# Kernel tuning notes

Hardware: AMD Instinct MI355X
Metric: run time of the kernel (lower is better)

## Reference

```python
import jax, jax.numpy as jnp
import numpy as np

K = 3
STRIDE = 1
PAD = 1
C_IN = 256
C_OUT = 256
BN_EPS = 1e-5


def conv2d(x, w, b, stride, pad):
    # x: (N,C,H,W), w: (O,I,K,K)
    y = jax.lax.conv_general_dilated(
        x, w, window_strides=(stride, stride),
        padding=((pad, pad), (pad, pad)),
        dimension_numbers=("NCHW", "OIHW", "NCHW"))
    return y + b[None, :, None, None]


def deform_conv2d(x, offset, weight, stride, pad, k):
    # torchvision-style deformable conv v1 (no modulation, no bias),
    # offset layout: (N, 2*k*k, Ho, Wo) with (dy, dx) pairs per kernel tap.
    N, C, H, W = x.shape
    Ho, Wo = offset.shape[2], offset.shape[3]
    KK = k * k
    off = offset.reshape(N, KK, 2, Ho, Wo)
    dy, dx = off[:, :, 0], off[:, :, 1]                      # (N,KK,Ho,Wo)

    ky, kx = jnp.meshgrid(jnp.arange(k), jnp.arange(k), indexing="ij")
    ky = ky.reshape(1, KK, 1, 1).astype(x.dtype)
    kx = kx.reshape(1, KK, 1, 1).astype(x.dtype)
    base_y = (jnp.arange(Ho) * stride - pad).astype(x.dtype)[None, None, :, None]
    base_x = (jnp.arange(Wo) * stride - pad).astype(x.dtype)[None, None, None, :]

    py = base_y + ky + dy                                     # (N,KK,Ho,Wo)
    px = base_x + kx + dx

    y0 = jnp.floor(py)
    x0 = jnp.floor(px)
    ly = py - y0
    lx = px - x0
    y0i = y0.astype(jnp.int32)
    x0i = x0.astype(jnp.int32)

    x_flat = x.reshape(N, C, H * W)

    def gather(yi, xi):
        valid = (yi >= 0) & (yi < H) & (xi >= 0) & (xi < W)
        yc = jnp.clip(yi, 0, H - 1)
        xc = jnp.clip(xi, 0, W - 1)
        idx = yc * W + xc                                     # (N,KK,Ho,Wo)
        v = jax.vmap(lambda xf, i: xf[:, i])(x_flat, idx)     # (N,C,KK,Ho,Wo)
        return v * valid[:, None].astype(x.dtype)

    w_tl = ((1 - ly) * (1 - lx))[:, None]
    w_tr = ((1 - ly) * lx)[:, None]
    w_bl = (ly * (1 - lx))[:, None]
    w_br = (ly * lx)[:, None]

    val = (w_tl * gather(y0i, x0i) + w_tr * gather(y0i, x0i + 1)
           + w_bl * gather(y0i + 1, x0i) + w_br * gather(y0i + 1, x0i + 1))
    # val: (N, Ci, KK, Ho, Wo); weight: (Co, Ci, k, k)
    w2 = weight.reshape(weight.shape[0], weight.shape[1], KK)
    return jnp.einsum("bikhw,oik->bohw", val, w2)


def setup_inputs() -> dict:
    key = jax.random.key(0)
    k1, k2, k3, k4 = jax.random.split(key, 4)
    N, H, W = 8, 64, 64
    x = jax.random.normal(k1, (N, C_IN, H, W), dtype=jnp.float32)
    # small nonzero offset-conv weights so the deformable gather is exercised
    w_offset = jax.random.normal(k2, (2 * K * K, C_IN, K, K), dtype=jnp.float32) * 0.01
    b_offset = jax.random.normal(k3, (2 * K * K,), dtype=jnp.float32) * 0.1
    w_conv = jax.random.normal(k4, (C_OUT, C_IN, K, K), dtype=jnp.float32) / np.sqrt(C_IN * K * K)
    gamma = jnp.ones((C_OUT,), dtype=jnp.float32)
    beta = jnp.zeros((C_OUT,), dtype=jnp.float32)
    return {"x": x, "w_offset": w_offset, "b_offset": b_offset,
            "w_conv": w_conv, "gamma": gamma, "beta": beta}


def reference(x, w_offset, b_offset, w_conv, gamma, beta):
    offset = conv2d(x, w_offset, b_offset, STRIDE, PAD)
    out = deform_conv2d(x, offset, w_conv, STRIDE, PAD, K)
    # BatchNorm2d in training mode: batch stats over (N,H,W), biased variance
    mean = jnp.mean(out, axis=(0, 2, 3), keepdims=True)
    var = jnp.mean(jnp.square(out - mean), axis=(0, 2, 3), keepdims=True)
    out = (out - mean) * jax.lax.rsqrt(var + BN_EPS)
    out = out * gamma[None, :, None, None] + beta[None, :, None, None]
    return out * jax.nn.sigmoid(out)  # SiLU
```

## Files before the change

### kernel.cpp

```cpp
#include <hip/hip_runtime.h>
#include <math.h>

#define HW 4096
#define KTOT 2304

typedef __attribute__((ext_vector_type(8))) short short8v;
typedef __attribute__((ext_vector_type(4))) float float4v;

__device__ __forceinline__ unsigned int bf16rne(float f) {
  unsigned int x = __float_as_uint(f);
  return (x + 0x7fffu + ((x >> 16) & 1u)) >> 16;
}

__device__ __forceinline__ unsigned int bilin_pack(unsigned int u0, unsigned int u1,
                                                   unsigned int u2, unsigned int u3,
                                                   float w0, float w1, float w2, float w3) {
  float lo = w0 * __uint_as_float(u0 << 16) + w1 * __uint_as_float(u1 << 16) +
             w2 * __uint_as_float(u2 << 16) + w3 * __uint_as_float(u3 << 16);
  float hi = w0 * __uint_as_float(u0 & 0xFFFF0000u) + w1 * __uint_as_float(u1 & 0xFFFF0000u) +
             w2 * __uint_as_float(u2 & 0xFFFF0000u) + w3 * __uint_as_float(u3 & 0xFFFF0000u);
  unsigned int r;
  asm("v_cvt_pk_bf16_f32 %0, %1, %2" : "=v"(r) : "v"(lo), "v"(hi));
  return r;
}


__global__ __launch_bounds__(256) void k_tx_prep(const float* __restrict__ x,
                                                 const float* __restrict__ wc,
                                                 const float* __restrict__ wo,
                                                 ushort* __restrict__ xT,
                                                 ushort* __restrict__ wB,
                                                 ushort* __restrict__ wOB) {
  int bid = blockIdx.x;
  if (bid < 512) {
    int n = bid & 7, p0 = (bid >> 3) << 6;
    int t = threadIdx.x;
    int lane = t & 63, wave = t >> 6, c0 = wave << 6;
    const float* xb = x + ((size_t)(n * 256 + c0)) * HW + p0 + lane;
    ushort* ob = xT + ((size_t)n * 4096 + p0 + lane) * 256 + c0;
#pragma unroll
    for (int g = 0; g < 8; ++g) {
      unsigned int u[4];
#pragma unroll
      for (int j = 0; j < 4; ++j) {
        float v0 = xb[(size_t)(g * 8 + 2 * j) * HW];
        float v1 = xb[(size_t)(g * 8 + 2 * j + 1) * HW];
        u[j] = bf16rne(v0) | (bf16rne(v1) << 16);
      }
      *reinterpret_cast<uint4*>(ob + g * 8) = make_uint4(u[0], u[1], u[2], u[3]);
    }
  } else if (bid < 800) {
    int t = (bid - 512) * 256 + threadIdx.x;
    int ks = t >> 10;
    int l = t & 63;
    int of = (t >> 6) & 15;
    int kk = ks >> 3;
    int cbase = ((ks & 7) << 5) + ((l >> 4) << 3);
    int oc = (of << 4) + (l & 15);
    unsigned int u[8];
#pragma unroll
    for (int j = 0; j < 8; ++j)
      u[j] = bf16rne(wc[(size_t)oc * KTOT + (size_t)(cbase + j) * 9 + kk]);
    *reinterpret_cast<uint4*>(&wB[(size_t)t * 8]) =
        make_uint4(u[0] | (u[1] << 16), u[2] | (u[3] << 16),
                   u[4] | (u[5] << 16), u[6] | (u[7] << 16));
  } else {
    int t = (bid - 800) * 256 + threadIdx.x;
    int ks = t >> 7;
    int l = t & 63;
    int of = (t >> 6) & 1;
    int kk = ks >> 3;
    int cbase = ((ks & 7) << 5) + ((l >> 4) << 3);
    int oc = (of << 4) + (l & 15);
    unsigned int u[8];
#pragma unroll
    for (int j = 0; j < 8; ++j)
      u[j] = (oc < 18) ? bf16rne(wo[(size_t)oc * KTOT + (size_t)(cbase + j) * 9 + kk]) : 0u;
    *reinterpret_cast<uint4*>(&wOB[(size_t)t * 8]) =
        make_uint4(u[0] | (u[1] << 16), u[2] | (u[3] << 16),
                   u[4] | (u[5] << 16), u[6] | (u[7] << 16));
  }
}

__global__ __launch_bounds__(512, 4) void k_offset5(
    const ushort* __restrict__ xT, const ushort* __restrict__ wOffB,
    const float* __restrict__ b_off, float* __restrict__ off_out) {
  __shared__ ushort s_tile[2][64 * 64];

  int bid = blockIdx.x;
  int n = bid & 7, ho = bid >> 3;
  int t = threadIdx.x;
  int lane = t & 63, wave = t >> 6;
  int coct = lane & 7;
  int p = (wave << 3) + (lane >> 3);
  int ocf = wave & 1, pixf = wave >> 1;

  const ushort* xTn = xT + (size_t)n * 4096 * 256;

  float4v acc = (float4v)0.f;

  auto srcp = [&](int kk, const ushort*& s, bool& v) {
    int ky = kk / 3, kx = kk - ky * 3;
    int oy = ho + ky - 1, ox = p + kx - 1;
    v = (oy >= 0) & (oy < 64) & (ox >= 0) & (ox < 64);
    s = xTn + (size_t)(oy * 64 + ox) * 256 + (coct << 3);
  };

  auto issue = [&](uint4& a, const ushort* s, bool v, int cg) {
    a = v ? *reinterpret_cast<const uint4*>(s + (cg << 6)) : make_uint4(0, 0, 0, 0);
  };

  auto step = [&](uint4 a, int ksb, int buf) {
    short8v wf[2];
#pragma unroll
    for (int ks2 = 0; ks2 < 2; ++ks2)
      wf[ks2] = *reinterpret_cast<const short8v*>(
          &wOffB[(((size_t)((ksb + ks2) * 2 + ocf)) * 64 + lane) * 8]);
    *reinterpret_cast<uint4*>(&s_tile[buf][p * 64 + ((coct ^ (p & 7)) << 3)]) = a;
    asm volatile("s_waitcnt lgkmcnt(0)" ::: "memory");
    __builtin_amdgcn_s_barrier();
#pragma unroll
    for (int ks2 = 0; ks2 < 2; ++ks2) {
      int row = (pixf << 4) + (lane & 15);
      int g = (ks2 << 2) + (lane >> 4);
      int slot = g ^ (row & 7);
      short8v vf = *reinterpret_cast<const short8v*>(&s_tile[buf][row * 64 + slot * 8]);
      acc = __builtin_amdgcn_mfma_f32_16x16x32_bf16(wf[ks2], vf, acc, 0, 0, 0);
    }
  };

  const ushort* cs;
  bool cv;
  srcp(0, cs, cv);
  uint4 A, B;
  issue(A, cs, cv, 0);

  for (int kk = 0; kk < 9; ++kk) {
    int ksb = kk << 3;
    issue(B, cs, cv, 1);
    step(A, ksb + 0, 0);
    issue(A, cs, cv, 2);
    step(B, ksb + 2, 1);
    issue(B, cs, cv, 3);
    step(A, ksb + 4, 0);
    const ushort* ns = cs;
    bool nv = cv;
    if (kk < 8) {
      srcp(kk + 1, ns, nv);
      issue(A, ns, nv, 0);
    }
    step(B, ksb + 6, 1);
    cs = ns; cv = nv;
  }

  int pixcol = (pixf << 4) + (lane & 15);
  size_t base = ((size_t)n * 4096 + ho * 64 + pixcol) * 18;
#pragma unroll
  for (int j = 0; j < 4; ++j) {
    int oc = (ocf << 4) + ((lane >> 4) << 2) + j;
    if (oc < 18) off_out[base + oc] = acc[j] + b_off[oc];
  }
}

__global__ __launch_bounds__(512, 4) void k_deform10(
    const ushort* __restrict__ xT, const float* __restrict__ off,
    const ushort* __restrict__ wB, float* __restrict__ out,
    float2* __restrict__ part) {
  __shared__ ushort s_val[2][64 * 64];
  __shared__ int4   s_gi[9][64];
  __shared__ float4 s_gw[9][64];

  int bid = blockIdx.x;
  int n = bid & 7, ho = bid >> 3;
  int t = threadIdx.x;
  int lane = t & 63, wave = t >> 6;
  int coct = lane & 7;
  int p = (wave << 3) + (lane >> 3);

  const ushort* xTn = xT + (size_t)n * 4096 * 256;

  for (int e = t; e < 576; e += 512) {
    int pix = e & 63, kk = e >> 6;
    int ky = kk / 3, kx = kk - ky * 3;
    const float* ob = off + ((size_t)n * 4096 + ho * 64 + pix) * 18;
    float dy = ob[2 * kk], dx = ob[2 * kk + 1];
    float py = (float)(ho - 1 + ky) + dy;
    float px = (float)(pix - 1 + kx) + dx;
    float y0f = floorf(py), x0f = floorf(px);
    float ly = py - y0f, lx = px - x0f;
    int y0 = (int)y0f, x0 = (int)x0f;
    int y1 = y0 + 1, x1 = x0 + 1;
    float vy0 = (y0 >= 0 && y0 < 64) ? 1.f : 0.f;
    float vy1 = (y1 >= 0 && y1 < 64) ? 1.f : 0.f;
    float vx0 = (x0 >= 0 && x0 < 64) ? 1.f : 0.f;
    float vx1 = (x1 >= 0 && x1 < 64) ? 1.f : 0.f;
    int cy0 = min(max(y0, 0), 63) << 6, cy1 = min(max(y1, 0), 63) << 6;
    int cx0 = min(max(x0, 0), 63), cx1 = min(max(x1, 0), 63);
    s_gi[kk][pix] = make_int4((cy0 + cx0) << 8, (cy0 + cx1) << 8,
                              (cy1 + cx0) << 8, (cy1 + cx1) << 8);
    s_gw[kk][pix] = make_float4((1.f - ly) * (1.f - lx) * vy0 * vx0,
                                (1.f - ly) * lx * vy0 * vx1,
                                ly * (1.f - lx) * vy1 * vx0,
                                ly * lx * vy1 * vx1);
  }
  __syncthreads();

  float4v acc[2][4];
#pragma unroll
  for (int a = 0; a < 2; ++a)
#pragma unroll
    for (int b = 0; b < 4; ++b) acc[a][b] = (float4v)0.f;

  uint4 TA[4], TB[4];

  auto issue = [&](uint4 (&T)[4], int kk, int cg) {
    int4 g = s_gi[kk][p];
    int cb = (cg << 6) + (coct << 3);
    T[0] = *reinterpret_cast<const uint4*>(xTn + g.x + cb);
    T[1] = *reinterpret_cast<const uint4*>(xTn + g.y + cb);
    T[2] = *reinterpret_cast<const uint4*>(xTn + g.z + cb);
    T[3] = *reinterpret_cast<const uint4*>(xTn + g.w + cb);
  };

  auto step = [&](uint4 (&T)[4], int kk, int ks0, int buf) {
    short8v wf[2][2];
#pragma unroll
    for (int ks2 = 0; ks2 < 2; ++ks2)
#pragma unroll
      for (int mf = 0; mf < 2; ++mf)
        wf[ks2][mf] = *reinterpret_cast<const short8v*>(
            &wB[(((size_t)((ks0 + ks2) * 16 + (wave << 1) + mf)) * 64 + lane) * 8]);
    float4 w = s_gw[kk][p];
    uint4 r;
    r.x = bilin_pack(T[0].x, T[1].x, T[2].x, T[3].x, w.x, w.y, w.z, w.w);
    r.y = bilin_pack(T[0].y, T[1].y, T[2].y, T[3].y, w.x, w.y, w.z, w.w);
    r.z = bilin_pack(T[0].z, T[1].z, T[2].z, T[3].z, w.x, w.y, w.z, w.w);
    r.w = bilin_pack(T[0].w, T[1].w, T[2].w, T[3].w, w.x, w.y, w.z, w.w);
    *reinterpret_cast<uint4*>(&s_val[buf][p * 64 + ((coct ^ (p & 7)) << 3)]) = r;
    asm volatile("s_waitcnt lgkmcnt(0)" ::: "memory");
    __builtin_amdgcn_s_barrier();
    __builtin_amdgcn_s_setprio(1);
#pragma unroll
    for (int ks2 = 0; ks2 < 2; ++ks2) {
#pragma unroll
      for (int pf = 0; pf < 4; ++pf) {
        int row = (pf << 4) + (lane & 15);
        int g = (ks2 << 2) + (lane >> 4);
        int slot = g ^ (row & 7);
        short8v vf = *reinterpret_cast<const short8v*>(&s_val[buf][row * 64 + slot * 8]);
#pragma unroll
        for (int mf = 0; mf < 2; ++mf)
          acc[mf][pf] = __builtin_amdgcn_mfma_f32_16x16x32_bf16(
              wf[ks2][mf], vf, acc[mf][pf], 0, 0, 0);
      }
    }
    __builtin_amdgcn_s_setprio(0);
  };

  issue(TA, 0, 0);
  for (int kk = 0; kk < 9; ++kk) {
    int ks0 = kk << 3;
    issue(TB, kk, 1);
    step(TA, kk, ks0 + 0, 0);
    issue(TA, kk, 2);
    step(TB, kk, ks0 + 2, 1);
    issue(TB, kk, 3);
    step(TA, kk, ks0 + 4, 0);
    if (kk < 8) issue(TA, kk + 1, 0);
    step(TB, kk, ks0 + 6, 1);
  }

#pragma unroll
  for (int mf = 0; mf < 2; ++mf) {
    int ocb = (wave << 5) + (mf << 4) + ((lane >> 4) << 2);
#pragma unroll
    for (int pf = 0; pf < 4; ++pf) {
      int wo = (pf << 4) + (lane & 15);
      float* op = out + (((size_t)(n * 256 + ocb)) * 64 + ho) * 64 + wo;
      float4v a = acc[mf][pf];
      op[0] = a[0];
      op[HW] = a[1];
      op[2 * HW] = a[2];
      op[3 * HW] = a[3];
    }
  }
  float s[2][4], q[2][4];
#pragma unroll
  for (int mf = 0; mf < 2; ++mf)
#pragma unroll
    for (int j = 0; j < 4; ++j) {
      float ss = 0.f, qq = 0.f;
#pragma unroll
      for (int pf = 0; pf < 4; ++pf) {
        float v = acc[mf][pf][j];
        ss += v;
        qq += v * v;
      }
      s[mf][j] = ss;
      q[mf][j] = qq;
    }
#pragma unroll
  for (int o = 1; o < 16; o <<= 1) {
#pragma unroll
    for (int mf = 0; mf < 2; ++mf)
#pragma unroll
      for (int j = 0; j < 4; ++j) {
        s[mf][j] += __shfl_xor(s[mf][j], o);
        q[mf][j] += __shfl_xor(q[mf][j], o);
      }
  }
  if ((lane & 15) == 0) {
#pragma unroll
    for (int mf = 0; mf < 2; ++mf)
#pragma unroll
      for (int j = 0; j < 4; ++j) {
        int oc = (wave << 5) + (mf << 4) + ((lane >> 4) << 2) + j;
        part[(size_t)oc * 512 + bid] = make_float2(s[mf][j], q[mf][j]);
      }
  }
}

__global__ __launch_bounds__(256) void k_stats_fin(const float2* __restrict__ part,
                                                   float2* __restrict__ stats) {
  int oc = blockIdx.x;
  int t = threadIdx.x;
  float2 a = part[(size_t)oc * 512 + t];
  float2 b = part[(size_t)oc * 512 + 256 + t];
  float s = a.x + b.x, q = a.y + b.y;
#pragma unroll
  for (int o = 32; o; o >>= 1) {
    s += __shfl_down(s, o);
    q += __shfl_down(q, o);
  }
  __shared__ float2 wsum[4];
  if ((t & 63) == 0) wsum[t >> 6] = make_float2(s, q);
  __syncthreads();
  if (t == 0) {
    float S = wsum[0].x + wsum[1].x + wsum[2].x + wsum[3].x;
    float Q = wsum[0].y + wsum[1].y + wsum[2].y + wsum[3].y;
    float mean = S / 32768.f;
    float var = Q / 32768.f - mean * mean;
    stats[oc] = make_float2(mean, rsqrtf(var + 1e-5f));
  }
}

__global__ __launch_bounds__(256) void k_bn_silu(float* __restrict__ out,
                                                 const float2* __restrict__ stats,
                                                 const float* __restrict__ gamma,
                                                 const float* __restrict__ beta) {
  int b = blockIdx.x;
  int nb = (b & 7) * 1024 + (b >> 3);
  size_t i4 = (size_t)nb * 256 + threadIdx.x;
  int ch = (int)((i4 >> 10) & 255);
  float2 st = stats[ch];
  float g = gamma[ch] * st.y;
  float bb = beta[ch] - st.x * g;
  float4 v = *(float4*)(out + i4 * 4);
  float y0 = v.x * g + bb, y1 = v.y * g + bb, y2 = v.z * g + bb, y3 = v.w * g + bb;
  v.x = y0 / (1.f + expf(-y0));
  v.y = y1 / (1.f + expf(-y1));
  v.z = y2 / (1.f + expf(-y2));
  v.w = y3 / (1.f + expf(-y3));
  *(float4*)(out + i4 * 4) = v;
}

extern "C" void kernel_launch(void* const* d_in, const int* in_sizes, int n_in,
                              void* d_out, int out_size, void* d_ws, size_t ws_size,
                              hipStream_t stream) {
  const float* x      = (const float*)d_in[0];
  const float* w_off  = (const float*)d_in[1];
  const float* b_off  = (const float*)d_in[2];
  const float* w_conv = (const float*)d_in[3];
  const float* gamma  = (const float*)d_in[4];
  const float* beta   = (const float*)d_in[5];
  float* out = (float*)d_out;

  float* ws       = (float*)d_ws;
  float*  ws_off  = ws;
  ushort* ws_xT   = (ushort*)(ws + 589824);
  ushort* ws_wB   = (ushort*)(ws + 4784128);
  ushort* ws_wOB  = (ushort*)(ws + 5079040);
  float2* ws_part = (float2*)(ws + 5115904);
  float2* ws_st   = (float2*)(ws + 5378048);

  k_tx_prep<<<836, 256, 0, stream>>>(x, w_conv, w_off, ws_xT, ws_wB, ws_wOB);
  k_offset5<<<512, 512, 0, stream>>>(ws_xT, ws_wOB, b_off, ws_off);
  k_deform10<<<512, 512, 0, stream>>>(ws_xT, ws_off, ws_wB, out, ws_part);
  k_stats_fin<<<256, 256, 0, stream>>>(ws_part, ws_st);
  k_bn_silu<<<8192, 256, 0, stream>>>(out, ws_st, gamma, beta);
}
```

Measured before the change: 108.4 us.

## Software-pipeline deform conv: pack next chunk while MFMAs consume previous buffer

Restructures the deformable-conv main loop into a flat 36-chunk pipeline. Each iteration packs bilinear values for chunk c into one LDS buffer while the MFMAs consume chunk c-1 from the other, with one barrier per chunk placed after both. Previously each step packed and then waited at a barrier before its own MFMAs. The aim is to overlap the gather/interpolation ALU work with matrix math and take the barrier wait off the critical path. The cost is more live registers and a prologue/epilogue.

Result: slower. 111.2 us (+2.5%).

```diff
diff --git a/kernel.cpp b/kernel.cpp
--- a/kernel.cpp
+++ b/kernel.cpp
@@ -162,7 +162,7 @@
   }
 }
 
-__global__ __launch_bounds__(512, 4) void k_deform10(
+__global__ __launch_bounds__(512, 4) void k_deform11(
     const ushort* __restrict__ xT, const float* __restrict__ off,
     const ushort* __restrict__ wB, float* __restrict__ out,
     float2* __restrict__ part) {
@@ -213,32 +213,26 @@
 
   uint4 TA[4], TB[4];
 
-  auto issue = [&](uint4 (&T)[4], int kk, int cg) {
-    int4 g = s_gi[kk][p];
-    int cb = (cg << 6) + (coct << 3);
+  auto issueT = [&](uint4 (&T)[4], int c) {
+    int4 g = s_gi[c >> 2][p];
+    int cb = ((c & 3) << 6) + (coct << 3);
     T[0] = *reinterpret_cast<const uint4*>(xTn + g.x + cb);
     T[1] = *reinterpret_cast<const uint4*>(xTn + g.y + cb);
     T[2] = *reinterpret_cast<const uint4*>(xTn + g.z + cb);
     T[3] = *reinterpret_cast<const uint4*>(xTn + g.w + cb);
   };
 
-  auto step = [&](uint4 (&T)[4], int kk, int ks0, int buf) {
-    short8v wf[2][2];
-#pragma unroll
-    for (int ks2 = 0; ks2 < 2; ++ks2)
-#pragma unroll
-      for (int mf = 0; mf < 2; ++mf)
-        wf[ks2][mf] = *reinterpret_cast<const short8v*>(
-            &wB[(((size_t)((ks0 + ks2) * 16 + (wave << 1) + mf)) * 64 + lane) * 8]);
-    float4 w = s_gw[kk][p];
+  auto pack = [&](uint4 (&T)[4], int c, int buf) {
+    float4 w = s_gw[c >> 2][p];
     uint4 r;
     r.x = bilin_pack(T[0].x, T[1].x, T[2].x, T[3].x, w.x, w.y, w.z, w.w);
     r.y = bilin_pack(T[0].y, T[1].y, T[2].y, T[3].y, w.x, w.y, w.z, w.w);
     r.z = bilin_pack(T[0].z, T[1].z, T[2].z, T[3].z, w.x, w.y, w.z, w.w);
     r.w = bilin_pack(T[0].w, T[1].w, T[2].w, T[3].w, w.x, w.y, w.z, w.w);
     *reinterpret_cast<uint4*>(&s_val[buf][p * 64 + ((coct ^ (p & 7)) << 3)]) = r;
-    asm volatile("s_waitcnt lgkmcnt(0)" ::: "memory");
-    __builtin_amdgcn_s_barrier();
+  };
+
+  auto mfma_exec = [&](short8v (&wf)[2][2], int buf) {
     __builtin_amdgcn_s_setprio(1);
 #pragma unroll
     for (int ks2 = 0; ks2 < 2; ++ks2) {
@@ -257,17 +251,47 @@
     __builtin_amdgcn_s_setprio(0);
   };
 
-  issue(TA, 0, 0);
-  for (int kk = 0; kk < 9; ++kk) {
-    int ks0 = kk << 3;
-    issue(TB, kk, 1);
-    step(TA, kk, ks0 + 0, 0);
-    issue(TA, kk, 2);
-    step(TB, kk, ks0 + 2, 1);
-    issue(TB, kk, 3);
-    step(TA, kk, ks0 + 4, 0);
-    if (kk < 8) issue(TA, kk + 1, 0);
-    step(TB, kk, ks0 + 6, 1);
+  auto load_wf = [&](short8v (&wf)[2][2], int m) {
+    int ks0 = m << 1;
+#pragma unroll
+    for (int ks2 = 0; ks2 < 2; ++ks2)
+#pragma unroll
+      for (int mf = 0; mf < 2; ++mf)
+        wf[ks2][mf] = *reinterpret_cast<const short8v*>(
+            &wB[(((size_t)((ks0 + ks2) * 16 + (wave << 1) + mf)) * 64 + lane) * 8]);
+  };
+
+  issueT(TA, 0);
+  issueT(TB, 1);
+  pack(TA, 0, 0);
+  asm volatile("s_waitcnt lgkmcnt(0)" ::: "memory");
+  __builtin_amdgcn_s_barrier();
+
+  for (int cc = 1; cc < 36; cc += 2) {
+    {
+      if (cc < 35) issueT(TA, cc + 1);
+      short8v wf[2][2];
+      load_wf(wf, cc - 1);
+      pack(TB, cc, 1);
+      mfma_exec(wf, 0);
+      asm volatile("s_waitcnt lgkmcnt(0)" ::: "memory");
+      __builtin_amdgcn_s_barrier();
+    }
+    if (cc + 1 < 36) {
+      if (cc + 2 < 36) issueT(TB, cc + 2);
+      short8v wf[2][2];
+      load_wf(wf, cc);
+      pack(TA, cc + 1, 0);
+      mfma_exec(wf, 1);
+      asm volatile("s_waitcnt lgkmcnt(0)" ::: "memory");
+      __builtin_amdgcn_s_barrier();
+    }
+  }
+
+  {
+    short8v wf[2][2];
+    load_wf(wf, 35);
+    mfma_exec(wf, 1);
   }
 
 #pragma unroll
@@ -385,7 +409,7 @@
 
   k_tx_prep<<<836, 256, 0, stream>>>(x, w_conv, w_off, ws_xT, ws_wB, ws_wOB);
   k_offset5<<<512, 512, 0, stream>>>(ws_xT, ws_wOB, b_off, ws_off);
-  k_deform10<<<512, 512, 0, stream>>>(ws_xT, ws_off, ws_wB, out, ws_part);
+  k_deform11<<<512, 512, 0, stream>>>(ws_xT, ws_off, ws_wB, out, ws_part);
   k_stats_fin<<<256, 256, 0, stream>>>(ws_part, ws_st);
   k_bn_silu<<<8192, 256, 0, stream>>>(out, ws_st, gamma, beta);
 }
```

## Stage two 64-channel chunks per barrier in deformable-conv main loop

Applied to the files above, without the earlier changes.

Restructures the deformable-conv main loop so each phase packs two 64-channel gathered tiles into a wider LDS buffer (128 channels per pixel) and runs two MFMA groups per barrier, halving the number of barriers from 36 to 18. It also issues gathers for the next phase before the current phase's weight loads and MFMAs, so global latency overlaps with compute. The cost is double the LDS for s_val (32 KB) and more live registers, which could lower occupancy under the 512x4 launch bound.

Result: no change. 108.6 us (+0.1%).

```diff
diff --git a/kernel.cpp b/kernel.cpp
--- a/kernel.cpp
+++ b/kernel.cpp
@@ -162,11 +162,11 @@
   }
 }
 
-__global__ __launch_bounds__(512, 4) void k_deform10(
+__global__ __launch_bounds__(512, 4) void k_deform12(
     const ushort* __restrict__ xT, const float* __restrict__ off,
     const ushort* __restrict__ wB, float* __restrict__ out,
     float2* __restrict__ part) {
-  __shared__ ushort s_val[2][64 * 64];
+  __shared__ ushort s_val[2][64 * 128];
   __shared__ int4   s_gi[9][64];
   __shared__ float4 s_gw[9][64];
 
@@ -213,33 +213,34 @@
 
   uint4 TA[4], TB[4];
 
-  auto issue = [&](uint4 (&T)[4], int kk, int cg) {
-    int4 g = s_gi[kk][p];
-    int cb = (cg << 6) + (coct << 3);
+  auto issueT = [&](uint4 (&T)[4], const int4& g, int c) {
+    int cb = ((c & 3) << 6) + (coct << 3);
     T[0] = *reinterpret_cast<const uint4*>(xTn + g.x + cb);
     T[1] = *reinterpret_cast<const uint4*>(xTn + g.y + cb);
     T[2] = *reinterpret_cast<const uint4*>(xTn + g.z + cb);
     T[3] = *reinterpret_cast<const uint4*>(xTn + g.w + cb);
   };
 
-  auto step = [&](uint4 (&T)[4], int kk, int ks0, int buf) {
-    short8v wf[2][2];
-#pragma unroll
-    for (int ks2 = 0; ks2 < 2; ++ks2)
-#pragma unroll
-      for (int mf = 0; mf < 2; ++mf)
-        wf[ks2][mf] = *reinterpret_cast<const short8v*>(
-            &wB[(((size_t)((ks0 + ks2) * 16 + (wave << 1) + mf)) * 64 + lane) * 8]);
-    float4 w = s_gw[kk][p];
+  auto pack = [&](uint4 (&T)[4], const float4& w, int c, int buf) {
     uint4 r;
     r.x = bilin_pack(T[0].x, T[1].x, T[2].x, T[3].x, w.x, w.y, w.z, w.w);
     r.y = bilin_pack(T[0].y, T[1].y, T[2].y, T[3].y, w.x, w.y, w.z, w.w);
     r.z = bilin_pack(T[0].z, T[1].z, T[2].z, T[3].z, w.x, w.y, w.z, w.w);
     r.w = bilin_pack(T[0].w, T[1].w, T[2].w, T[3].w, w.x, w.y, w.z, w.w);
-    *reinterpret_cast<uint4*>(&s_val[buf][p * 64 + ((coct ^ (p & 7)) << 3)]) = r;
-    asm volatile("s_waitcnt lgkmcnt(0)" ::: "memory");
-    __builtin_amdgcn_s_barrier();
-    __builtin_amdgcn_s_setprio(1);
+    *reinterpret_cast<uint4*>(
+        &s_val[buf][p * 128 + ((c & 1) << 6) + ((coct ^ (p & 7)) << 3)]) = r;
+  };
+
+  auto load_wf2 = [&](short8v (&wf)[2][2], int ksbase) {
+#pragma unroll
+    for (int ks2 = 0; ks2 < 2; ++ks2)
+#pragma unroll
+      for (int mf = 0; mf < 2; ++mf)
+        wf[ks2][mf] = *reinterpret_cast<const short8v*>(
+            &wB[(((size_t)((ksbase + ks2) * 16 + (wave << 1) + mf)) * 64 + lane) * 8]);
+  };
+
+  auto mfma2 = [&](short8v (&wf)[2][2], int buf, int half) {
 #pragma unroll
     for (int ks2 = 0; ks2 < 2; ++ks2) {
 #pragma unroll
@@ -247,27 +248,43 @@
         int row = (pf << 4) + (lane & 15);
         int g = (ks2 << 2) + (lane >> 4);
         int slot = g ^ (row & 7);
-        short8v vf = *reinterpret_cast<const short8v*>(&s_val[buf][row * 64 + slot * 8]);
+        short8v vf = *reinterpret_cast<const short8v*>(
+            &s_val[buf][row * 128 + (half << 6) + slot * 8]);
 #pragma unroll
         for (int mf = 0; mf < 2; ++mf)
           acc[mf][pf] = __builtin_amdgcn_mfma_f32_16x16x32_bf16(
               wf[ks2][mf], vf, acc[mf][pf], 0, 0, 0);
       }
     }
+  };
+
+  {
+    int4 g0 = s_gi[0][p];
+    issueT(TA, g0, 0);
+    issueT(TB, g0, 1);
+  }
+
+  for (int ph = 0; ph < 18; ++ph) {
+    int kk = ph >> 1;
+    int buf = ph & 1;
+    float4 w = s_gw[kk][p];
+    pack(TA, w, 2 * ph, buf);
+    pack(TB, w, 2 * ph + 1, buf);
+    if (ph < 17) {
+      int4 g = s_gi[(ph + 1) >> 1][p];
+      issueT(TA, g, 2 * ph + 2);
+      issueT(TB, g, 2 * ph + 3);
+    }
+    short8v wf01[2][2];
+    load_wf2(wf01, 4 * ph);
+    asm volatile("s_waitcnt lgkmcnt(0)" ::: "memory");
+    __builtin_amdgcn_s_barrier();
+    short8v wf23[2][2];
+    load_wf2(wf23, 4 * ph + 2);
+    __builtin_amdgcn_s_setprio(1);
+    mfma2(wf01, buf, 0);
+    mfma2(wf23, buf, 1);
     __builtin_amdgcn_s_setprio(0);
-  };
-
-  issue(TA, 0, 0);
-  for (int kk = 0; kk < 9; ++kk) {
-    int ks0 = kk << 3;
-    issue(TB, kk, 1);
-    step(TA, kk, ks0 + 0, 0);
-    issue(TA, kk, 2);
-    step(TB, kk, ks0 + 2, 1);
-    issue(TB, kk, 3);
-    step(TA, kk, ks0 + 4, 0);
-    if (kk < 8) issue(TA, kk + 1, 0);
-    step(TB, kk, ks0 + 6, 1);
   }
 
 #pragma unroll
@@ -385,7 +402,7 @@
 
   k_tx_prep<<<836, 256, 0, stream>>>(x, w_conv, w_off, ws_xT, ws_wB, ws_wOB);
   k_offset5<<<512, 512, 0, stream>>>(ws_xT, ws_wOB, b_off, ws_off);
-  k_deform10<<<512, 512, 0, stream>>>(ws_xT, ws_off, ws_wB, out, ws_part);
+  k_deform12<<<512, 512, 0, stream>>>(ws_xT, ws_off, ws_wB, out, ws_part);
   k_stats_fin<<<256, 256, 0, stream>>>(ws_part, ws_st);
   k_bn_silu<<<8192, 256, 0, stream>>>(out, ws_st, gamma, beta);
 }
```

## Fuse offset conv into deformable conv kernel and stage transpose through LDS

Applied to the files above, without the earlier changes.

The offset-prediction conv is merged into the deformable conv kernel. Each block computes its own row of 18 offset channels with MFMA, keeps them in shared memory, and reuses the s_val buffer, so one launch and the global round trip for offsets go away. The x transpose in the prep kernel now goes through an LDS tile with padding, which makes the bf16 global stores coalesced and uses the hardware packed convert. The trade-off is more shared memory and registers per block in the fused kernel, which could lower occupancy, plus a block-wide sync between the offset and deform phases.

Result: faster. 102.9 us, median of 2 (-5.1%).

```diff
diff --git a/kernel.cpp b/kernel.cpp
--- a/kernel.cpp
+++ b/kernel.cpp
@@ -10,6 +10,12 @@
 __device__ __forceinline__ unsigned int bf16rne(float f) {
   unsigned int x = __float_as_uint(f);
   return (x + 0x7fffu + ((x >> 16) & 1u)) >> 16;
+}
+
+__device__ __forceinline__ unsigned int cvtpk(float lo, float hi) {
+  unsigned int r;
+  asm("v_cvt_pk_bf16_f32 %0, %1, %2" : "=v"(r) : "v"(lo), "v"(hi));
+  return r;
 }
 
 __device__ __forceinline__ unsigned int bilin_pack(unsigned int u0, unsigned int u1,
@@ -19,9 +25,7 @@
              w2 * __uint_as_float(u2 << 16) + w3 * __uint_as_float(u3 << 16);
   float hi = w0 * __uint_as_float(u0 & 0xFFFF0000u) + w1 * __uint_as_float(u1 & 0xFFFF0000u) +
              w2 * __uint_as_float(u2 & 0xFFFF0000u) + w3 * __uint_as_float(u3 & 0xFFFF0000u);
-  unsigned int r;
-  asm("v_cvt_pk_bf16_f32 %0, %1, %2" : "=v"(r) : "v"(lo), "v"(hi));
-  return r;
+  return cvtpk(lo, hi);
 }
 
 
@@ -31,23 +35,30 @@
                                                  ushort* __restrict__ xT,
                                                  ushort* __restrict__ wB,
                                                  ushort* __restrict__ wOB) {
+  __shared__ unsigned s32[64 * 129];
   int bid = blockIdx.x;
   if (bid < 512) {
     int n = bid & 7, p0 = (bid >> 3) << 6;
     int t = threadIdx.x;
-    int lane = t & 63, wave = t >> 6, c0 = wave << 6;
-    const float* xb = x + ((size_t)(n * 256 + c0)) * HW + p0 + lane;
-    ushort* ob = xT + ((size_t)n * 4096 + p0 + lane) * 256 + c0;
-#pragma unroll
-    for (int g = 0; g < 8; ++g) {
-      unsigned int u[4];
-#pragma unroll
-      for (int j = 0; j < 4; ++j) {
-        float v0 = xb[(size_t)(g * 8 + 2 * j) * HW];
-        float v1 = xb[(size_t)(g * 8 + 2 * j + 1) * HW];
-        u[j] = bf16rne(v0) | (bf16rne(v1) << 16);
-      }
-      *reinterpret_cast<uint4*>(ob + g * 8) = make_uint4(u[0], u[1], u[2], u[3]);
+    int pixr = t & 63;
+    int cq = t >> 6;
+    const float* xb = x + ((size_t)n * 256) * HW + p0 + pixr;
+#pragma unroll 4
+    for (int g = 0; g < 32; ++g) {
+      int c0 = (g << 3) + (cq << 1);
+      float v0 = xb[(size_t)c0 * HW];
+      float v1 = xb[(size_t)(c0 + 1) * HW];
+      s32[pixr * 129 + (c0 >> 1)] = cvtpk(v0, v1);
+    }
+    __syncthreads();
+    int cslot = t & 31;
+    int pw = t >> 5;
+#pragma unroll
+    for (int pass = 0; pass < 8; ++pass) {
+      int pix = (pass << 3) + pw;
+      uint4 v = *reinterpret_cast<const uint4*>(&s32[pix * 129 + (cslot << 2)]);
+      *reinterpret_cast<uint4*>(
+          &xT[((size_t)(n * 4096 + p0 + pix)) * 256 + (cslot << 3)]) = v;
     }
   } else if (bid < 800) {
     int t = (bid - 512) * 256 + threadIdx.x;
@@ -82,10 +93,14 @@
   }
 }
 
-__global__ __launch_bounds__(512, 4) void k_offset5(
-    const ushort* __restrict__ xT, const ushort* __restrict__ wOffB,
-    const float* __restrict__ b_off, float* __restrict__ off_out) {
-  __shared__ ushort s_tile[2][64 * 64];
+__global__ __launch_bounds__(512, 4) void k_dfull(
+    const ushort* __restrict__ xT, const ushort* __restrict__ wB,
+    const ushort* __restrict__ wOB, const float* __restrict__ b_off,
+    float* __restrict__ out, float2* __restrict__ part) {
+  __shared__ ushort s_val[2][64 * 64];
+  __shared__ int4   s_gi[9][64];
+  __shared__ float4 s_gw[9][64];
+  __shared__ float  s_off[64][20];
 
   int bid = blockIdx.x;
   int n = bid & 7, ho = bid >> 3;
@@ -93,97 +108,77 @@
   int lane = t & 63, wave = t >> 6;
   int coct = lane & 7;
   int p = (wave << 3) + (lane >> 3);
-  int ocf = wave & 1, pixf = wave >> 1;
 
   const ushort* xTn = xT + (size_t)n * 4096 * 256;
 
-  float4v acc = (float4v)0.f;
-
-  auto srcp = [&](int kk, const ushort*& s, bool& v) {
-    int ky = kk / 3, kx = kk - ky * 3;
-    int oy = ho + ky - 1, ox = p + kx - 1;
-    v = (oy >= 0) & (oy < 64) & (ox >= 0) & (ox < 64);
-    s = xTn + (size_t)(oy * 64 + ox) * 256 + (coct << 3);
-  };
-
-  auto issue = [&](uint4& a, const ushort* s, bool v, int cg) {
-    a = v ? *reinterpret_cast<const uint4*>(s + (cg << 6)) : make_uint4(0, 0, 0, 0);
-  };
-
-  auto step = [&](uint4 a, int ksb, int buf) {
-    short8v wf[2];
-#pragma unroll
-    for (int ks2 = 0; ks2 < 2; ++ks2)
-      wf[ks2] = *reinterpret_cast<const short8v*>(
-          &wOffB[(((size_t)((ksb + ks2) * 2 + ocf)) * 64 + lane) * 8]);
-    *reinterpret_cast<uint4*>(&s_tile[buf][p * 64 + ((coct ^ (p & 7)) << 3)]) = a;
-    asm volatile("s_waitcnt lgkmcnt(0)" ::: "memory");
-    __builtin_amdgcn_s_barrier();
-#pragma unroll
-    for (int ks2 = 0; ks2 < 2; ++ks2) {
-      int row = (pixf << 4) + (lane & 15);
-      int g = (ks2 << 2) + (lane >> 4);
-      int slot = g ^ (row & 7);
-      short8v vf = *reinterpret_cast<const short8v*>(&s_tile[buf][row * 64 + slot * 8]);
-      acc = __builtin_amdgcn_mfma_f32_16x16x32_bf16(wf[ks2], vf, acc, 0, 0, 0);
-    }
-  };
-
-  const ushort* cs;
-  bool cv;
-  srcp(0, cs, cv);
-  uint4 A, B;
-  issue(A, cs, cv, 0);
-
-  for (int kk = 0; kk < 9; ++kk) {
-    int ksb = kk << 3;
-    issue(B, cs, cv, 1);
-    step(A, ksb + 0, 0);
-    issue(A, cs, cv, 2);
-    step(B, ksb + 2, 1);
-    issue(B, cs, cv, 3);
-    step(A, ksb + 4, 0);
-    const ushort* ns = cs;
-    bool nv = cv;
-    if (kk < 8) {
-      srcp(kk + 1, ns, nv);
-      issue(A, ns, nv, 0);
-    }
-    step(B, ksb + 6, 1);
-    cs = ns; cv = nv;
-  }
-
-  int pixcol = (pixf << 4) + (lane & 15);
-  size_t base = ((size_t)n * 4096 + ho * 64 + pixcol) * 18;
-#pragma unroll
-  for (int j = 0; j < 4; ++j) {
-    int oc = (ocf << 4) + ((lane >> 4) << 2) + j;
-    if (oc < 18) off_out[base + oc] = acc[j] + b_off[oc];
-  }
-}
-
-__global__ __launch_bounds__(512, 4) void k_deform10(
-    const ushort* __restrict__ xT, const float* __restrict__ off,
-    const ushort* __restrict__ wB, float* __restrict__ out,
-    float2* __restrict__ part) {
-  __shared__ ushort s_val[2][64 * 64];
-  __shared__ int4   s_gi[9][64];
-  __shared__ float4 s_gw[9][64];
-
-  int bid = blockIdx.x;
-  int n = bid & 7, ho = bid >> 3;
-  int t = threadIdx.x;
-  int lane = t & 63, wave = t >> 6;
-  int coct = lane & 7;
-  int p = (wave << 3) + (lane >> 3);
-
-  const ushort* xTn = xT + (size_t)n * 4096 * 256;
+  {
+    int ocf = wave & 1, pixf = wave >> 1;
+    float4v aoff = (float4v)0.f;
+
+    auto srcp = [&](int kk, const ushort*& s, bool& v) {
+      int ky = kk / 3, kx = kk - ky * 3;
+      int oy = ho + ky - 1, ox = p + kx - 1;
+      v = (oy >= 0) & (oy < 64) & (ox >= 0) & (ox < 64);
+      s = xTn + (size_t)(oy * 64 + ox) * 256 + (coct << 3);
+    };
+    auto ld = [&](uint4& a, const ushort* s, bool v, int cg) {
+      a = v ? *reinterpret_cast<const uint4*>(s + (cg << 6)) : make_uint4(0, 0, 0, 0);
+    };
+    auto ostep = [&](uint4 a, int ksb, int buf) {
+      short8v wf[2];
+#pragma unroll
+      for (int ks2 = 0; ks2 < 2; ++ks2)
+        wf[ks2] = *reinterpret_cast<const short8v*>(
+            &wOB[(((size_t)((ksb + ks2) * 2 + ocf)) * 64 + lane) * 8]);
+      *reinterpret_cast<uint4*>(&s_val[buf][p * 64 + ((coct ^ (p & 7)) << 3)]) = a;
+      asm volatile("s_waitcnt lgkmcnt(0)" ::: "memory");
+      __builtin_amdgcn_s_barrier();
+#pragma unroll
+      for (int ks2 = 0; ks2 < 2; ++ks2) {
+        int row = (pixf << 4) + (lane & 15);
+        int g = (ks2 << 2) + (lane >> 4);
+        int slot = g ^ (row & 7);
+        short8v vf = *reinterpret_cast<const short8v*>(&s_val[buf][row * 64 + slot * 8]);
+        aoff = __builtin_amdgcn_mfma_f32_16x16x32_bf16(wf[ks2], vf, aoff, 0, 0, 0);
+      }
+    };
+
+    const ushort* cs;
+    bool cv;
+    srcp(0, cs, cv);
+    uint4 A, B;
+    ld(A, cs, cv, 0);
+    for (int kk = 0; kk < 9; ++kk) {
+      int ksb = kk << 3;
+      ld(B, cs, cv, 1);
+      ostep(A, ksb + 0, 0);
+      ld(A, cs, cv, 2);
+      ostep(B, ksb + 2, 1);
+      ld(B, cs, cv, 3);
+      ostep(A, ksb + 4, 0);
+      const ushort* ns = cs;
+      bool nv = cv;
+      if (kk < 8) {
+        srcp(kk + 1, ns, nv);
+        ld(A, ns, nv, 0);
+      }
+      ostep(B, ksb + 6, 1);
+      cs = ns;
+      cv = nv;
+    }
+    int pixcol = (pixf << 4) + (lane & 15);
+#pragma unroll
+    for (int j = 0; j < 4; ++j) {
+      int oc = (ocf << 4) + ((lane >> 4) << 2) + j;
+      if (oc < 18) s_off[pixcol][oc] = aoff[j] + b_off[oc];
+    }
+  }
+  __syncthreads();
 
   for (int e = t; e < 576; e += 512) {
     int pix = e & 63, kk = e >> 6;
     int ky = kk / 3, kx = kk - ky * 3;
-    const float* ob = off + ((size_t)n * 4096 + ho * 64 + pix) * 18;
-    float dy = ob[2 * kk], dx = ob[2 * kk + 1];
+    float dy = s_off[pix][2 * kk], dx = s_off[pix][2 * kk + 1];
     float py = (float)(ho - 1 + ky) + dy;
     float px = (float)(pix - 1 + kx) + dx;
     float y0f = floorf(py), x0f = floorf(px);
@@ -376,7 +371,6 @@
   float* out = (float*)d_out;
 
   float* ws       = (float*)d_ws;
-  float*  ws_off  = ws;
   ushort* ws_xT   = (ushort*)(ws + 589824);
   ushort* ws_wB   = (ushort*)(ws + 4784128);
   ushort* ws_wOB  = (ushort*)(ws + 5079040);
@@ -384,8 +378,7 @@
   float2* ws_st   = (float2*)(ws + 5378048);
 
   k_tx_prep<<<836, 256, 0, stream>>>(x, w_conv, w_off, ws_xT, ws_wB, ws_wOB);
-  k_offset5<<<512, 512, 0, stream>>>(ws_xT, ws_wOB, b_off, ws_off);
-  k_deform10<<<512, 512, 0, stream>>>(ws_xT, ws_off, ws_wB, out, ws_part);
+  k_dfull<<<512, 512, 0, stream>>>(ws_xT, ws_wB, ws_wOB, b_off, out, ws_part);
   k_stats_fin<<<256, 256, 0, stream>>>(ws_part, ws_st);
   k_bn_silu<<<8192, 256, 0, stream>>>(out, ws_st, gamma, beta);
 }
```
